# Kernel tuning notes

Measured on AMD Instinct MI355X. Metric: run time of the kernel, lower is better.

Reference implementation:

```python
import jax, jax.numpy as jnp
import numpy as np

N, L, D = 8, 2048, 128


def setup_inputs() -> dict:
    key = jax.random.key(0)
    k1, k2, k3, k4 = jax.random.split(key, 4)
    x_t = jax.random.normal(k1, (N, L, D), jnp.float32)
    x_f = jax.random.normal(k2, (N, L, D), jnp.float32)
    W = jax.random.normal(k3, (D, D), jnp.float32) / np.sqrt(D)  # proj weight (torch Linear layout)
    b = jax.random.normal(k4, (D,), jnp.float32) * 0.02
    return {"x_t": x_t, "x_f": x_f, "W": W, "b": b}


def _col_score(a, c, scale):
    # softmax attention with zeroed diagonal, then column-sum -> [N, L]
    att = jnp.einsum('nld,nmd->nlm', a, c) * scale
    att = jax.nn.softmax(att, axis=-1)
    att = att * (1.0 - jnp.eye(att.shape[-1], dtype=att.dtype))
    return jnp.sum(att, axis=1)


def _mask(score, time):
    # score: [N, L]; k-th extreme threshold, k = L//2
    k = int(0.5 * score.shape[1])
    if time:
        vals, _ = jax.lax.top_k(score, k)          # k largest, descending
        theta = vals[:, -1:]                        # k-th largest
        return score > theta
    else:
        vals, _ = jax.lax.top_k(-score, k)          # k smallest
        theta = -vals[:, -1:]                       # k-th smallest
        return score <= theta


def reference(x_t, x_f, W, b):
    scale = 1.0 / np.sqrt(W.shape[0])
    pt = x_t @ W.T + b
    pf = x_f @ W.T + b
    score_t = _col_score(pt, pt, scale)
    score_f = _col_score(pf, pf, scale)
    score_tf = _col_score(pt, pf, scale)
    score_ft = _col_score(pf, pt, scale)
    mask_t = _mask(score_t, False)
    mask_f = _mask(score_f, False)
    mask_tf = _mask(score_tf, True)   # computed in original forward (unused in blend)
    mask_ft = _mask(score_ft, True)
    mask_t1 = (mask_t & ~mask_f)[:, :, None]   # [N, L, 1] broadcast over D
    mask_f1 = (mask_f & ~mask_t)[:, :, None]
    x_t1 = jnp.where(mask_t1, x_f, x_t)
    x_f1 = jnp.where(mask_f1, x_t, x_f)
    return (0.5 * (x_t1 + x_t), 0.5 * (x_f1 + x_f))
```

## Files before the change

kernel.cpp:

```cpp
#include <hip/hip_runtime.h>
#include <math.h>

#define LL 2048
#define DD 128
#define NS 16
#define SLAB (LL * DD)
#define SCALE 0.08838834764831845f

typedef __attribute__((ext_vector_type(8))) short short8v;
typedef __attribute__((ext_vector_type(4))) float float4v;

__device__ __forceinline__ unsigned int f2bf(float f) {
    unsigned int u = __float_as_uint(f);
    u += 0x7fffu + ((u >> 16) & 1u);
    return u >> 16;
}

__device__ __forceinline__ void strip_decode(int bx, int by, int& ib, int& ns) {
    const int lin = by * 16 + bx;
    const int xcd = lin & 7;
    const int w   = lin >> 3;
    ns = xcd + 8 * (w & 1);
    ib = w >> 1;
}

__device__ __forceinline__ void gl_lds16(const void* g, void* l) {
    __builtin_amdgcn_global_load_lds(
        (const __attribute__((address_space(1))) void*)g,
        (__attribute__((address_space(3))) void*)l, 16, 0, 0);
}

__device__ __forceinline__ void stage512(
    const unsigned short* __restrict__ gT, unsigned short* lbuf, int tid)
{
    const int row = tid >> 2;
    const int oc  = (tid & 3) ^ ((row >> 1) & 3);
    const int sb  = tid & ~63;
    gl_lds16(gT + (size_t)row * DD + oc * 8, lbuf + (size_t)sb * 8);
}

#define STAGE_HALF(DST, GH, GL, KC) do {                       \
    stage512((GH) + (KC) * 32,       (DST)[0], tid);           \
    stage512((GL) + (KC) * 32,       (DST)[1], tid);           \
    stage512((GH) + ((KC) + 1) * 32, (DST)[2], tid);           \
    stage512((GL) + ((KC) + 1) * 32, (DST)[3], tid); } while (0)

#define ZEROACC(ACC) do {                                      \
    _Pragma("unroll") for (int rt = 0; rt < 4; ++rt)           \
    _Pragma("unroll") for (int ct = 0; ct < 2; ++ct)           \
    _Pragma("unroll") for (int r = 0; r < 4; ++r) (ACC)[rt][ct][r] = 0.f; } while (0)

#define KC2(ACC, CB, KI, AKC) do {                                           \
    const unsigned short* BhP = (CB)[2 * (KI)];                              \
    const unsigned short* BlP = (CB)[2 * (KI) + 1];                          \
    short8v bh[2], bl[2];                                                    \
    _Pragma("unroll")                                                        \
    for (int ct = 0; ct < 2; ++ct) {                                         \
        const int r = wc * 32 + ct * 16 + l16;                               \
        const int off = r * 32 + ((quad ^ ((r >> 1) & 3)) << 3);             \
        bh[ct] = *(const short8v*)&BhP[off];                                 \
        bl[ct] = *(const short8v*)&BlP[off];                                 \
    }                                                                        \
    __builtin_amdgcn_s_setprio(1);                                           \
    _Pragma("unroll")                                                        \
    for (int rt = 0; rt < 4; ++rt)                                           \
    _Pragma("unroll")                                                        \
    for (int ct = 0; ct < 2; ++ct) {                                         \
        (ACC)[rt][ct] = __builtin_amdgcn_mfma_f32_16x16x32_bf16(ah[AKC][rt], bh[ct], (ACC)[rt][ct], 0, 0, 0); \
        (ACC)[rt][ct] = __builtin_amdgcn_mfma_f32_16x16x32_bf16(ah[AKC][rt], bl[ct], (ACC)[rt][ct], 0, 0, 0); \
        (ACC)[rt][ct] = __builtin_amdgcn_mfma_f32_16x16x32_bf16(alr[AKC][rt], bh[ct], (ACC)[rt][ct], 0, 0, 0); \
    }                                                                        \
    __builtin_amdgcn_s_setprio(0); } while (0)

#define EPI1(ACC) do {                                         \
    _Pragma("unroll") for (int rt = 0; rt < 4; ++rt)           \
    _Pragma("unroll") for (int rg = 0; rg < 4; ++rg) {         \
        float e0 = __expf((ACC)[rt][0][rg] * SCALE);           \
        float e1 = __expf((ACC)[rt][1][rg] * SCALE);           \
        z[rt][rg] += e0 + e1; } } while (0)

#define EPI2(ACC, JBV) do {                                    \
    float colp0 = 0.f, colp1 = 0.f;                            \
    const bool dgj = ((JBV) == ib);                            \
    _Pragma("unroll") for (int rt = 0; rt < 4; ++rt)           \
    _Pragma("unroll") for (int rg = 0; rg < 4; ++rg) {         \
        const int rl = wr * 64 + rt * 16 + quad * 4 + rg;      \
        float e0 = __expf((ACC)[rt][0][rg] * SCALE);           \
        float e1 = __expf((ACC)[rt][1][rg] * SCALE);           \
        bool s0 = dgj && (rl == wc * 32 + l16);                \
        bool s1 = dgj && (rl == wc * 32 + 16 + l16);           \
        colp0 += s0 ? 0.f : e0 * wrow[rt][rg];                 \
        colp1 += s1 ? 0.f : e1 * wrow[rt][rg]; }               \
    colp0 += __shfl_xor(colp0, 16); colp0 += __shfl_xor(colp0, 32); \
    colp1 += __shfl_xor(colp1, 16); colp1 += __shfl_xor(colp1, 32); \
    if (quad == 0) {                                           \
        scs[(JBV) * 128 + wc * 32 + l16][wr]      = colp0;     \
        scs[(JBV) * 128 + wc * 32 + 16 + l16][wr] = colp1; } } while (0)

__global__ __launch_bounds__(512) void proj_kernel(
    const float* __restrict__ xt, const float* __restrict__ xf,
    const float* __restrict__ W,  const float* __restrict__ bias,
    unsigned short* __restrict__ Ph, unsigned short* __restrict__ Pl)
{
    __shared__ float Wl[128 * 128];
    __shared__ float Xl[128 * 128];
    const int ns = blockIdx.y;
    const int l0 = blockIdx.x * 128;
    const int src = ns >> 3, n = ns & 7;
    const float* x = (src ? xf : xt) + (size_t)n * LL * DD + (size_t)l0 * DD;
    const int tid = threadIdx.x;
    const int ty = tid >> 4, tx = tid & 15;

#pragma unroll
    for (int it = 0; it < 8; ++it) {
        const int s   = it * 512 + tid;
        const int row = s >> 5, c = s & 31;
        const int oc  = c ^ (row & 7);
        const int sb  = it * 512 + (tid & ~63);
        gl_lds16(W + (size_t)row * DD + oc * 4, Wl + (size_t)sb * 4);
        gl_lds16(x + (size_t)row * DD + oc * 4, Xl + (size_t)sb * 4);
    }

    float acc[4][8];
#pragma unroll
    for (int i = 0; i < 4; ++i)
#pragma unroll
        for (int j = 0; j < 8; ++j) acc[i][j] = bias[tx + 16 * j];

    __syncthreads();

    const int rs = ty & 7, ds = tx & 7;
#pragma unroll 4
    for (int k4 = 0; k4 < 128; k4 += 4) {
        const int c = k4 >> 2;
        float4 xv[4], wv[8];
#pragma unroll
        for (int i = 0; i < 4; ++i)
            xv[i] = *(const float4*)&Xl[(ty + 32 * i) * 128 + ((c ^ rs) << 2)];
#pragma unroll
        for (int j = 0; j < 8; ++j)
            wv[j] = *(const float4*)&Wl[(tx + 16 * j) * 128 + ((c ^ ds) << 2)];
#pragma unroll
        for (int i = 0; i < 4; ++i)
#pragma unroll
            for (int j = 0; j < 8; ++j) {
                acc[i][j] = fmaf(xv[i].x, wv[j].x, acc[i][j]);
                acc[i][j] = fmaf(xv[i].y, wv[j].y, acc[i][j]);
                acc[i][j] = fmaf(xv[i].z, wv[j].z, acc[i][j]);
                acc[i][j] = fmaf(xv[i].w, wv[j].w, acc[i][j]);
            }
    }

#pragma unroll
    for (int i = 0; i < 4; ++i) {
        const size_t rowo = (size_t)ns * SLAB + (size_t)(l0 + ty + 32 * i) * DD;
#pragma unroll
        for (int j = 0; j < 8; ++j) {
            float p = acc[i][j];
            unsigned int hb = f2bf(p);
            float hf = __uint_as_float(hb << 16);
            unsigned int lb = f2bf(p - hf);
            Ph[rowo + tx + 16 * j] = (unsigned short)hb;
            Pl[rowo + tx + 16 * j] = (unsigned short)lb;
        }
    }
}

__global__ __launch_bounds__(512, 1) void score_kernel(
    const unsigned short* __restrict__ Ph, const unsigned short* __restrict__ Pl,
    float* __restrict__ Spart)
{
    __shared__ unsigned short pan[2][4][4096];
    __shared__ float scs[2048][2];
    __shared__ float zl[128][4];
    int ib, ns;  strip_decode(blockIdx.x, blockIdx.y, ib, ns);
    const int tid = threadIdx.x;
    const int lane = tid & 63, quad = lane >> 4, l16 = lane & 15, wave = tid >> 6;
    const int wr = wave >> 2, wc = wave & 3;

    const unsigned short* sAh = Ph + (size_t)ns * SLAB + (size_t)ib * 128 * DD;
    const unsigned short* sAl = Pl + (size_t)ns * SLAB + (size_t)ib * 128 * DD;
    const unsigned short* sBh = Ph + (size_t)ns * SLAB;
    const unsigned short* sBl = Pl + (size_t)ns * SLAB;

    short8v alr[4][4];
#pragma unroll
    for (int kc = 0; kc < 4; ++kc)
#pragma unroll
        for (int rt = 0; rt < 4; ++rt)
            alr[kc][rt] = *(const short8v*)
                &sAl[(size_t)(wr * 64 + rt * 16 + l16) * DD + kc * 32 + quad * 8];
#pragma unroll
    for (int kc = 0; kc < 4; ++kc)
#pragma unroll
        for (int rt = 0; rt < 4; ++rt)
            asm volatile("" : "+v"(alr[kc][rt]));

    STAGE_HALF(pan[0], sBh, sBl, 0);
    short8v ah[4][4];
#pragma unroll
    for (int kc = 0; kc < 4; ++kc)
#pragma unroll
        for (int rt = 0; rt < 4; ++rt)
            ah[kc][rt] = *(const short8v*)
                &sAh[(size_t)(wr * 64 + rt * 16 + l16) * DD + kc * 32 + quad * 8];
    __syncthreads();

    float4v accA[4][2], accB[4][2];
    float z[4][4];
#pragma unroll
    for (int rt = 0; rt < 4; ++rt)
#pragma unroll
        for (int rg = 0; rg < 4; ++rg) z[rt][rg] = 0.f;

#pragma unroll 1
    for (int jp = 0; jp < 8; ++jp) {
        const unsigned short* b0h = sBh + (size_t)(2 * jp) * 128 * DD;
        const unsigned short* b0l = sBl + (size_t)(2 * jp) * 128 * DD;
        const unsigned short* b1h = b0h + 128 * DD;
        const unsigned short* b1l = b0l + 128 * DD;
        const unsigned short* b2h = b1h + 128 * DD;
        const unsigned short* b2l = b1l + 128 * DD;

        ZEROACC(accA);
        STAGE_HALF(pan[1], b0h, b0l, 2);
        KC2(accA, pan[0], 0, 0);
        KC2(accA, pan[0], 1, 1);
        if (jp) EPI1(accB);
        __syncthreads();

        STAGE_HALF(pan[0], b1h, b1l, 0);
        KC2(accA, pan[1], 0, 2);
        KC2(accA, pan[1], 1, 3);
        __syncthreads();

        ZEROACC(accB);
        STAGE_HALF(pan[1], b1h, b1l, 2);
        KC2(accB, pan[0], 0, 0);
        KC2(accB, pan[0], 1, 1);
        EPI1(accA);
        __syncthreads();

        if (jp < 7) STAGE_HALF(pan[0], b2h, b2l, 0);
        KC2(accB, pan[1], 0, 2);
        KC2(accB, pan[1], 1, 3);
        __syncthreads();
    }
    EPI1(accB);

#pragma unroll
    for (int rt = 0; rt < 4; ++rt)
#pragma unroll
        for (int rg = 0; rg < 4; ++rg) {
            float s = z[rt][rg];
            s += __shfl_xor(s, 1);
            s += __shfl_xor(s, 2);
            s += __shfl_xor(s, 4);
            s += __shfl_xor(s, 8);
            if (l16 == 0) zl[wr * 64 + rt * 16 + quad * 4 + rg][wc] = s;
        }
    STAGE_HALF(pan[0], sBh, sBl, 0);
    __syncthreads();
    float wrow[4][4];
#pragma unroll
    for (int rt = 0; rt < 4; ++rt)
#pragma unroll
        for (int rg = 0; rg < 4; ++rg) {
            const int row = wr * 64 + rt * 16 + quad * 4 + rg;
            wrow[rt][rg] = 1.0f / (zl[row][0] + zl[row][1] + zl[row][2] + zl[row][3]);
        }

#pragma unroll 1
    for (int jp = 0; jp < 8; ++jp) {
        const unsigned short* b0h = sBh + (size_t)(2 * jp) * 128 * DD;
        const unsigned short* b0l = sBl + (size_t)(2 * jp) * 128 * DD;
        const unsigned short* b1h = b0h + 128 * DD;
        const unsigned short* b1l = b0l + 128 * DD;
        const unsigned short* b2h = b1h + 128 * DD;
        const unsigned short* b2l = b1l + 128 * DD;

        ZEROACC(accA);
        STAGE_HALF(pan[1], b0h, b0l, 2);
        KC2(accA, pan[0], 0, 0);
        KC2(accA, pan[0], 1, 1);
        if (jp) EPI2(accB, 2 * jp - 1);
        __syncthreads();

        STAGE_HALF(pan[0], b1h, b1l, 0);
        KC2(accA, pan[1], 0, 2);
        KC2(accA, pan[1], 1, 3);
        __syncthreads();

        ZEROACC(accB);
        STAGE_HALF(pan[1], b1h, b1l, 2);
        KC2(accB, pan[0], 0, 0);
        KC2(accB, pan[0], 1, 1);
        EPI2(accA, 2 * jp);
        __syncthreads();

        if (jp < 7) STAGE_HALF(pan[0], b2h, b2l, 0);
        KC2(accB, pan[1], 0, 2);
        KC2(accB, pan[1], 1, 3);
        __syncthreads();
    }
    EPI2(accB, 15);

    __syncthreads();
#pragma unroll
    for (int g = 0; g < 4; ++g) {
        const int m = tid + g * 512;
        Spart[((size_t)ns * LL + m) * 16 + ib] = scs[m][0] + scs[m][1];
    }
}

__global__ __launch_bounds__(512) void mask_kernel(
    const float* __restrict__ Spart, unsigned char* __restrict__ maskbuf)
{
    __shared__ double s[LL];
    const int ns = blockIdx.x;
    const int q4 = blockIdx.y;
    const int tid = threadIdx.x;
#pragma unroll
    for (int g = 0; g < 4; ++g) {
        int m = tid + g * 512;
        const float* sp = Spart + ((size_t)ns * LL + m) * 16;
        double a = 0.0;
#pragma unroll
        for (int t = 0; t < 16; ++t) a += (double)sp[t];
        s[m] = a;
    }
    __syncthreads();
    const int i = q4 * 512 + tid;
    const double si = s[i];
    const double2* sv = (const double2*)s;
    int cnt = 0;
#pragma unroll 4
    for (int j = 0; j < LL / 2; ++j) {
        double2 p = sv[j];
        cnt += (p.x < si) ? 1 : 0;
        cnt += (p.y < si) ? 1 : 0;
    }
    maskbuf[ns * LL + i] = (cnt < 1024) ? 1 : 0;
}

__global__ __launch_bounds__(256) void blend_kernel(
    const float* __restrict__ xt, const float* __restrict__ xf,
    const unsigned char* __restrict__ maskbuf, float* __restrict__ out)
{
    const int idx4 = blockIdx.x * 256 + threadIdx.x;
    const size_t q = (size_t)idx4 * 4;
    const int row = (int)(q >> 7);
    const float4 a = *(const float4*)(xt + q);
    const float4 b = *(const float4*)(xf + q);
    const int mt = maskbuf[row] & 1;
    const int mf = maskbuf[16384 + row] & 1;
    const bool ct = mt && !mf;
    const bool cf = mf && !mt;
    float4 av;
    av.x = 0.5f * (a.x + b.x);  av.y = 0.5f * (a.y + b.y);
    av.z = 0.5f * (a.z + b.z);  av.w = 0.5f * (a.w + b.w);
    float4 o0 = ct ? av : a;
    float4 o1 = cf ? av : b;
    *(float4*)(out + q)                   = o0;
    *(float4*)(out + (size_t)2097152 + q) = o1;
}

extern "C" void kernel_launch(void* const* d_in, const int* in_sizes, int n_in,
                              void* d_out, int out_size, void* d_ws, size_t ws_size,
                              hipStream_t stream)
{
    const float* xt = (const float*)d_in[0];
    const float* xf = (const float*)d_in[1];
    const float* W  = (const float*)d_in[2];
    const float* b  = (const float*)d_in[3];
    float* out = (float*)d_out;

    unsigned short* Ph = (unsigned short*)d_out;
    unsigned short* Pl = Ph + (size_t)NS * SLAB;

    float* Spart = (float*)d_ws;
    unsigned char* maskbuf = (unsigned char*)(Spart + (size_t)16 * LL * 16);

    proj_kernel<<<dim3(16, NS), 512, 0, stream>>>(xt, xf, W, b, Ph, Pl);
    score_kernel<<<dim3(16, 16), 512, 0, stream>>>(Ph, Pl, Spart);
    mask_kernel<<<dim3(NS, 4), 512, 0, stream>>>(Spart, maskbuf);
    blend_kernel<<<2048, 256, 0, stream>>>(xt, xf, maskbuf, out);
}
```

Baseline: 225.9 us.

## Move A-low fragments from registers to LDS to allow two blocks per CU

The low-half bf16 A fragments that were held in registers for the whole kernel are now staged once into a shared-memory panel and reloaded from LDS inside each MFMA step. The MFMA sequence is regrouped into three passes (hi×hi, hi×lo, lo×hi), and launch bounds are raised to request two 512-thread blocks per CU. The aim is to free VGPRs so occupancy doubles and latency hides better. In exchange the kernel does extra LDS reads per step and uses more shared memory, which may stop two blocks from fitting or cause LDS bank pressure.

```diff
diff --git a/kernel.cpp b/kernel.cpp
--- a/kernel.cpp
+++ b/kernel.cpp
@@ -53,7 +53,7 @@
 #define KC2(ACC, CB, KI, AKC) do {                                           \
     const unsigned short* BhP = (CB)[2 * (KI)];                              \
     const unsigned short* BlP = (CB)[2 * (KI) + 1];                          \
-    short8v bh[2], bl[2];                                                    \
+    short8v bh[2], bl[2], alv[4];                                            \
     _Pragma("unroll")                                                        \
     for (int ct = 0; ct < 2; ++ct) {                                         \
         const int r = wc * 32 + ct * 16 + l16;                               \
@@ -61,15 +61,28 @@
         bh[ct] = *(const short8v*)&BhP[off];                                 \
         bl[ct] = *(const short8v*)&BlP[off];                                 \
     }                                                                        \
+    _Pragma("unroll")                                                        \
+    for (int rt = 0; rt < 4; ++rt) {                                         \
+        const int r = wr * 64 + rt * 16 + l16;                               \
+        const int off = r * 32 + ((quad ^ ((r >> 1) & 3)) << 3);             \
+        alv[rt] = *(const short8v*)&Alpan[AKC][off];                         \
+    }                                                                        \
     __builtin_amdgcn_s_setprio(1);                                           \
     _Pragma("unroll")                                                        \
     for (int rt = 0; rt < 4; ++rt)                                           \
     _Pragma("unroll")                                                        \
-    for (int ct = 0; ct < 2; ++ct) {                                         \
+    for (int ct = 0; ct < 2; ++ct)                                           \
         (ACC)[rt][ct] = __builtin_amdgcn_mfma_f32_16x16x32_bf16(ah[AKC][rt], bh[ct], (ACC)[rt][ct], 0, 0, 0); \
+    _Pragma("unroll")                                                        \
+    for (int rt = 0; rt < 4; ++rt)                                           \
+    _Pragma("unroll")                                                        \
+    for (int ct = 0; ct < 2; ++ct)                                           \
         (ACC)[rt][ct] = __builtin_amdgcn_mfma_f32_16x16x32_bf16(ah[AKC][rt], bl[ct], (ACC)[rt][ct], 0, 0, 0); \
-        (ACC)[rt][ct] = __builtin_amdgcn_mfma_f32_16x16x32_bf16(alr[AKC][rt], bh[ct], (ACC)[rt][ct], 0, 0, 0); \
-    }                                                                        \
+    _Pragma("unroll")                                                        \
+    for (int rt = 0; rt < 4; ++rt)                                           \
+    _Pragma("unroll")                                                        \
+    for (int ct = 0; ct < 2; ++ct)                                           \
+        (ACC)[rt][ct] = __builtin_amdgcn_mfma_f32_16x16x32_bf16(alv[rt], bh[ct], (ACC)[rt][ct], 0, 0, 0); \
     __builtin_amdgcn_s_setprio(0); } while (0)
 
 #define EPI1(ACC) do {                                         \
@@ -166,11 +179,12 @@
     }
 }
 
-__global__ __launch_bounds__(512, 1) void score_kernel(
+__global__ __launch_bounds__(512, 2) void score_kernel(
     const unsigned short* __restrict__ Ph, const unsigned short* __restrict__ Pl,
     float* __restrict__ Spart)
 {
     __shared__ unsigned short pan[2][4][4096];
+    __shared__ unsigned short Alpan[4][4096];
     __shared__ float scs[2048][2];
     __shared__ float zl[128][4];
     int ib, ns;  strip_decode(blockIdx.x, blockIdx.y, ib, ns);
@@ -183,19 +197,10 @@
     const unsigned short* sBh = Ph + (size_t)ns * SLAB;
     const unsigned short* sBl = Pl + (size_t)ns * SLAB;
 
-    short8v alr[4][4];
-#pragma unroll
-    for (int kc = 0; kc < 4; ++kc)
-#pragma unroll
-        for (int rt = 0; rt < 4; ++rt)
-            alr[kc][rt] = *(const short8v*)
-                &sAl[(size_t)(wr * 64 + rt * 16 + l16) * DD + kc * 32 + quad * 8];
-#pragma unroll
-    for (int kc = 0; kc < 4; ++kc)
-#pragma unroll
-        for (int rt = 0; rt < 4; ++rt)
-            asm volatile("" : "+v"(alr[kc][rt]));
-
+    stage512(sAl,      Alpan[0], tid);
+    stage512(sAl + 32, Alpan[1], tid);
+    stage512(sAl + 64, Alpan[2], tid);
+    stage512(sAl + 96, Alpan[3], tid);
     STAGE_HALF(pan[0], sBh, sBl, 0);
     short8v ah[4][4];
 #pragma unroll
```

Result: faster. 221.3 us (-2.1%).
